# Performance work log

Hardware: AMD Instinct MI355X
Metric: run time of the kernel (lower is better)

## Reference

```python
import jax, jax.numpy as jnp
import numpy as np

N = 50000
E = 800000
IN_CH = 128
HIDDEN = 32
HEADS = 4
OUT_CH = 64
NEG_SLOPE = 0.2


def setup_inputs() -> dict:
    key = jax.random.key(0)
    ks = jax.random.split(key, 12)
    x = jax.random.normal(ks[0], (N, IN_CH), dtype=jnp.float32)
    edge_index = jax.random.randint(ks[1], (2, E), 0, N, dtype=jnp.int64)
    # layer 1: GATConv(IN_CH, HIDDEN, heads=4, concat=True)
    s1 = 1.0 / np.sqrt(IN_CH)
    W1 = jax.random.normal(ks[2], (IN_CH, HEADS * HIDDEN), dtype=jnp.float32) * s1
    att_src1 = jax.random.normal(ks[3], (HEADS, HIDDEN), dtype=jnp.float32) * 0.1
    att_dst1 = jax.random.normal(ks[4], (HEADS, HIDDEN), dtype=jnp.float32) * 0.1
    b1 = jnp.zeros((HEADS * HIDDEN,), dtype=jnp.float32)
    # layer 2: GATConv(HEADS*HIDDEN, OUT_CH, heads=1, concat=False)
    s2 = 1.0 / np.sqrt(HEADS * HIDDEN)
    W2 = jax.random.normal(ks[5], (HEADS * HIDDEN, OUT_CH), dtype=jnp.float32) * s2
    att_src2 = jax.random.normal(ks[6], (1, OUT_CH), dtype=jnp.float32) * 0.1
    att_dst2 = jax.random.normal(ks[7], (1, OUT_CH), dtype=jnp.float32) * 0.1
    b2 = jnp.zeros((OUT_CH,), dtype=jnp.float32)
    return {"x": x, "edge_index": edge_index, "W1": W1, "att_src1": att_src1,
            "att_dst1": att_dst1, "b1": b1, "W2": W2, "att_src2": att_src2,
            "att_dst2": att_dst2, "b2": b2}


def gat_conv(x, src, dst, W, a_src, a_dst, bias, heads, out_ch, concat):
    n = x.shape[0]
    h = (x @ W).reshape(n, heads, out_ch)               # [N, H, C]
    alpha_s = jnp.sum(h * a_src[None], axis=-1)          # [N, H]
    alpha_d = jnp.sum(h * a_dst[None], axis=-1)          # [N, H]
    e = alpha_s[src] + alpha_d[dst]                      # [E, H]
    e = jnp.where(e > 0, e, NEG_SLOPE * e)               # leaky_relu(0.2)
    # segment softmax over incoming edges of each dst node
    e_max = jax.ops.segment_max(e, dst, num_segments=n)
    e_max = jnp.where(jnp.isfinite(e_max), e_max, 0.0)
    ex = jnp.exp(e - e_max[dst])
    denom = jax.ops.segment_sum(ex, dst, num_segments=n)
    alpha = ex / (denom[dst] + 1e-16)                    # [E, H]
    msg = h[src] * alpha[:, :, None]                     # [E, H, C]
    out = jax.ops.segment_sum(msg, dst, num_segments=n)  # [N, H, C]
    if concat:
        out = out.reshape(n, heads * out_ch)
    else:
        out = out.mean(axis=1)
    return out + bias


def reference(x, edge_index, W1, att_src1, att_dst1, b1, W2, att_src2, att_dst2, b2):
    n = x.shape[0]
    loop = jnp.arange(n, dtype=edge_index.dtype)
    src = jnp.concatenate([edge_index[0], loop])  # add self-loops (PyG default)
    dst = jnp.concatenate([edge_index[1], loop])
    h = gat_conv(x, src, dst, W1, att_src1, att_dst1, b1, HEADS, HIDDEN, True)
    h = jax.nn.elu(h)
    return gat_conv(h, src, dst, W2, att_src2, att_dst2, b2, 1, OUT_CH, False)
```

## Files before the change

### kernel.cpp

```cpp
#include <hip/hip_runtime.h>

#define NN    50000
#define NE    800000
#define NET   850000
#define NBUCK ((NN + 255) / 256)
#define MAXB  8192

typedef __fp16 half2_t __attribute__((ext_vector_type(2)));
typedef _Float16 half8 __attribute__((ext_vector_type(8)));
typedef float floatx4 __attribute__((ext_vector_type(4)));

__device__ __forceinline__ float lrelu(float v) { return fmaxf(v, 0.2f * v); }
__device__ __forceinline__ unsigned pk16(float a, float b) {
    half2_t h = __builtin_amdgcn_cvt_pkrtz(a, b);
    return __builtin_bit_cast(unsigned, h);
}
__device__ __forceinline__ float2 unpk16(unsigned u) {
    half2_t h = __builtin_bit_cast(half2_t, u);
    return make_float2((float)h.x, (float)h.y);
}

__global__ void prep_w_kernel(const float* __restrict__ W1, const float* __restrict__ W2,
                              _Float16* __restrict__ w1t, _Float16* __restrict__ w2t)
{
    const int idx = blockIdx.x * 256 + threadIdx.x;
    if (idx < 16384) {
        const int k = idx >> 7, n = idx & 127;
        w1t[n * 128 + k] = (_Float16)W1[idx];
    } else {
        const int j = idx - 16384;
        const int k = j >> 6, n = j & 63;
        w2t[n * 128 + k] = (_Float16)W2[j];
    }
}

__global__ __launch_bounds__(256) void gemm1_mfma_kernel(
    const float* __restrict__ x, const _Float16* __restrict__ w1t,
    const float* __restrict__ att_s, const float* __restrict__ att_d,
    _Float16* __restrict__ h1h, float* __restrict__ as, float* __restrict__ ad)
{
    __shared__ _Float16 hs[64 * 128];
    const int t    = threadIdx.x;
    const int lane = t & 63;
    const int m    = lane & 15;
    const int q    = lane >> 4;
    const int wv   = t >> 6;
    const int gr0  = blockIdx.x * 64;
    const int rbase = gr0 + wv * 16;

    const int rme = rbase + m;
    const int rc  = rme < NN ? rme : NN - 1;
    const float* ap = x + (size_t)rc * 128 + q * 8;

    floatx4 acc[8];
#pragma unroll
    for (int nt = 0; nt < 8; nt++) acc[nt] = (floatx4){0.f, 0.f, 0.f, 0.f};

#pragma unroll
    for (int ks = 0; ks < 4; ks++) {
        const float4 f0 = *(const float4*)(ap + ks * 32);
        const float4 f1 = *(const float4*)(ap + ks * 32 + 4);
        const uint4 au = make_uint4(pk16(f0.x, f0.y), pk16(f0.z, f0.w),
                                    pk16(f1.x, f1.y), pk16(f1.z, f1.w));
        const half8 a = __builtin_bit_cast(half8, au);
#pragma unroll
        for (int nt = 0; nt < 8; nt++) {
            const half8 b = *(const half8*)(w1t + (nt * 16 + m) * 128 + ks * 32 + q * 8);
            acc[nt] = __builtin_amdgcn_mfma_f32_16x16x32_f16(a, b, acc[nt], 0, 0, 0);
        }
    }

    const int lrow0 = wv * 16 + q * 4;
#pragma unroll
    for (int nt = 0; nt < 8; nt++)
#pragma unroll
        for (int r = 0; r < 4; r++)
            hs[(lrow0 + r) * 128 + nt * 16 + m] = (_Float16)acc[nt][r];
    __syncthreads();

#pragma unroll
    for (int i = t; i < 1024; i += 256) {
        const int row = i >> 4;
        if (gr0 + row < NN)
            ((half8*)h1h)[(size_t)(gr0 + row) * 16 + (i & 15)] = ((const half8*)hs)[i];
    }

    const int arow = t >> 2, hd = t & 3;
    const int grow = gr0 + arow;
    float ps = 0.f, pd = 0.f;
    const half8*  hp8 = (const half8*)(hs + arow * 128 + hd * 32);
    const float4* s4  = (const float4*)(att_s + hd * 32);
    const float4* d4  = (const float4*)(att_d + hd * 32);
#pragma unroll
    for (int cc = 0; cc < 4; cc++) {
        const half8 hv = hp8[cc];
        const float4 a = s4[cc * 2], b = s4[cc * 2 + 1];
        const float4 c = d4[cc * 2], e = d4[cc * 2 + 1];
        ps += (float)hv[0]*a.x + (float)hv[1]*a.y + (float)hv[2]*a.z + (float)hv[3]*a.w
            + (float)hv[4]*b.x + (float)hv[5]*b.y + (float)hv[6]*b.z + (float)hv[7]*b.w;
        pd += (float)hv[0]*c.x + (float)hv[1]*c.y + (float)hv[2]*c.z + (float)hv[3]*c.w
            + (float)hv[4]*e.x + (float)hv[5]*e.y + (float)hv[6]*e.z + (float)hv[7]*e.w;
    }
    if (grow < NN) {
        as[grow * 4 + hd] = ps;
        ad[grow * 4 + hd] = pd;
    }
}

__global__ __launch_bounds__(256) void gemm2_mfma_kernel(
    const _Float16* __restrict__ ah, const _Float16* __restrict__ w2t,
    const float* __restrict__ att_s, const float* __restrict__ att_d,
    _Float16* __restrict__ h2h, float* __restrict__ as, float* __restrict__ ad)
{
    __shared__ _Float16 hs[64 * 64];
    const int t    = threadIdx.x;
    const int lane = t & 63;
    const int m    = lane & 15;
    const int q    = lane >> 4;
    const int wv   = t >> 6;
    const int gr0  = blockIdx.x * 64;
    const int rbase = gr0 + wv * 16;

    const int rme = rbase + m;
    const int rc  = rme < NN ? rme : NN - 1;
    const _Float16* ap = ah + (size_t)rc * 128 + q * 8;

    floatx4 acc[4];
#pragma unroll
    for (int nt = 0; nt < 4; nt++) acc[nt] = (floatx4){0.f, 0.f, 0.f, 0.f};

#pragma unroll
    for (int ks = 0; ks < 4; ks++) {
        const half8 a = *(const half8*)(ap + ks * 32);
#pragma unroll
        for (int nt = 0; nt < 4; nt++) {
            const half8 b = *(const half8*)(w2t + (nt * 16 + m) * 128 + ks * 32 + q * 8);
            acc[nt] = __builtin_amdgcn_mfma_f32_16x16x32_f16(a, b, acc[nt], 0, 0, 0);
        }
    }

    const int lrow0 = wv * 16 + q * 4;
#pragma unroll
    for (int nt = 0; nt < 4; nt++)
#pragma unroll
        for (int r = 0; r < 4; r++)
            hs[(lrow0 + r) * 64 + nt * 16 + m] = (_Float16)acc[nt][r];
    __syncthreads();

#pragma unroll
    for (int i = t; i < 512; i += 256) {
        const int row = i >> 3;
        if (gr0 + row < NN)
            ((half8*)h2h)[(size_t)(gr0 + row) * 8 + (i & 7)] = ((const half8*)hs)[i];
    }

    const int arow = t >> 2, sg = t & 3;
    const int grow = gr0 + arow;
    float ps = 0.f, pd = 0.f;
    const half8*  hp8 = (const half8*)(hs + arow * 64 + sg * 16);
    const float4* s4  = (const float4*)(att_s + sg * 16);
    const float4* d4  = (const float4*)(att_d + sg * 16);
#pragma unroll
    for (int cc = 0; cc < 2; cc++) {
        const half8 hv = hp8[cc];
        const float4 a = s4[cc * 2], b = s4[cc * 2 + 1];
        const float4 c = d4[cc * 2], e = d4[cc * 2 + 1];
        ps += (float)hv[0]*a.x + (float)hv[1]*a.y + (float)hv[2]*a.z + (float)hv[3]*a.w
            + (float)hv[4]*b.x + (float)hv[5]*b.y + (float)hv[6]*b.z + (float)hv[7]*b.w;
        pd += (float)hv[0]*c.x + (float)hv[1]*c.y + (float)hv[2]*c.z + (float)hv[3]*c.w
            + (float)hv[4]*e.x + (float)hv[5]*e.y + (float)hv[6]*e.z + (float)hv[7]*e.w;
    }
    ps += __shfl_down(ps, 2);  pd += __shfl_down(pd, 2);
    ps += __shfl_down(ps, 1);  pd += __shfl_down(pd, 1);
    if (sg == 0 && grow < NN) { as[grow] = ps; ad[grow] = pd; }
}

__global__ __launch_bounds__(1024) void bin_kernel(const int* __restrict__ ei,
                                                   int* __restrict__ bcnt,
                                                   uint2* __restrict__ pairs)
{
    __shared__ int hist[NBUCK], base[NBUCK], cur[NBUCK];
    const int t = threadIdx.x;
    if (t < NBUCK) { hist[t] = 0; cur[t] = 0; }
    __syncthreads();
    const int e = blockIdx.x * 1024 + t;
    int s = 0, d = 0, bk = 0;
    const bool ok = e < NET;
    if (ok) {
        if (e < NE) { s = ei[e]; d = ei[NE + e]; } else { s = d = e - NE; }
        bk = d >> 8;
        atomicAdd(&hist[bk], 1);
    }
    __syncthreads();
    if (t < NBUCK && hist[t]) base[t] = atomicAdd(&bcnt[t], hist[t]);
    __syncthreads();
    if (ok) {
        const int r = atomicAdd(&cur[bk], 1);
        pairs[(size_t)bk * MAXB + base[bk] + r] = make_uint2((unsigned)s, (unsigned)d);
    }
}

__global__ __launch_bounds__(512) void bsort_ew1_kernel(
    const int* __restrict__ bcnt, const uint2* __restrict__ pairs,
    const float* __restrict__ as1, const float* __restrict__ ad1,
    int* __restrict__ row_beg, int* __restrict__ row_end,
    int* __restrict__ col, int* __restrict__ cold, float4* __restrict__ ex1)
{
    __shared__ int hist[256], cur[256], sh[256];
    __shared__ int outl[MAXB];
    __shared__ int outd[MAXB];
    const int b = blockIdx.x, t = threadIdx.x;
    const int m = bcnt[b];
    const int gbase = b * MAXB;
    if (t < 256) hist[t] = 0;
    __syncthreads();
    for (int i = t; i < m; i += 512)
        atomicAdd(&hist[pairs[gbase + i].y & 255], 1);
    __syncthreads();
    if (t < 256) sh[t] = hist[t];
    __syncthreads();
#pragma unroll
    for (int off = 1; off < 256; off <<= 1) {
        int u = (t < 256 && t >= off) ? sh[t - off] : 0;
        __syncthreads();
        if (t < 256) sh[t] += u;
        __syncthreads();
    }
    if (t < 256) {
        const int ex = sh[t] - hist[t];
        cur[t] = ex;
        const int node = (b << 8) + t;
        if (node < NN) {
            row_beg[node] = gbase + ex;
            row_end[node] = gbase + ex + hist[t];
        }
    }
    __syncthreads();
    for (int i = t; i < m; i += 512) {
        const uint2 p = pairs[gbase + i];
        const int r = atomicAdd(&cur[p.y & 255], 1);
        outl[r] = (int)p.x;
        outd[r] = (int)p.y;
    }
    __syncthreads();
    for (int i = t; i < m; i += 512) {
        const int s = outl[i], dd = outd[i];
        col[gbase + i]  = s;
        cold[gbase + i] = dd;
        const float4 a = ((const float4*)as1)[s];
        const float4 bb = ((const float4*)ad1)[dd];
        float4 v;
        v.x = __expf(lrelu(a.x + bb.x));
        v.y = __expf(lrelu(a.y + bb.y));
        v.z = __expf(lrelu(a.z + bb.z));
        v.w = __expf(lrelu(a.w + bb.w));
        ex1[gbase + i] = v;
    }
}

__global__ void edge_w2_kernel(const int* __restrict__ bcnt,
                               const int* __restrict__ col, const int* __restrict__ cold,
                               const float* __restrict__ as, const float* __restrict__ ad,
                               float* __restrict__ ex)
{
    const int bk    = blockIdx.x >> 5;
    const int local = (blockIdx.x & 31) * 256 + threadIdx.x;
    if (local >= bcnt[bk]) return;
    const int j = bk * MAXB + local;
    ex[j] = __expf(lrelu(as[col[j]] + ad[cold[j]]));
}

__global__ __launch_bounds__(256) void agg1_fused_kernel(
    const int* __restrict__ row_beg, const int* __restrict__ row_end,
    const int* __restrict__ col, const unsigned* __restrict__ hh,
    const float* __restrict__ exw, const float* __restrict__ b1,
    unsigned* __restrict__ acth)
{
    const int d    = __builtin_amdgcn_readfirstlane((blockIdx.x * 256 + threadIdx.x) >> 6);
    const int lane = threadIdx.x & 63;
    const int head = lane >> 4;
    const int beg = row_beg[d], end = row_end[d];

    float acc0 = 0.f, acc1 = 0.f, den = 0.f;
    int j = beg;
    for (; j + 16 <= end; j += 16) {
        float    w[16];
        unsigned g[16];
#pragma unroll
        for (int k = 0; k < 16; k++) {
            const int s = col[j + k];
            w[k] = exw[(j + k) * 4 + head];
            g[k] = hh[s * 64 + lane];
        }
#pragma unroll
        for (int k = 0; k < 16; k++) {
            const float2 g2 = unpk16(g[k]);
            den  += w[k];
            acc0 += w[k] * g2.x;
            acc1 += w[k] * g2.y;
        }
    }
    for (; j + 4 <= end; j += 4) {
        float    w[4];
        unsigned g[4];
#pragma unroll
        for (int k = 0; k < 4; k++) {
            const int s = col[j + k];
            w[k] = exw[(j + k) * 4 + head];
            g[k] = hh[s * 64 + lane];
        }
#pragma unroll
        for (int k = 0; k < 4; k++) {
            const float2 g2 = unpk16(g[k]);
            den  += w[k];
            acc0 += w[k] * g2.x;
            acc1 += w[k] * g2.y;
        }
    }
    for (; j < end; j++) {
        const float w = exw[j * 4 + head];
        const float2 g2 = unpk16(hh[col[j] * 64 + lane]);
        den  += w;
        acc0 += w * g2.x;
        acc1 += w * g2.y;
    }
    const float2 bb  = ((const float2*)b1)[lane];
    const float  inv = 1.f / (den + 1e-16f);
    float v0 = acc0 * inv + bb.x;
    float v1 = acc1 * inv + bb.y;
    v0 = v0 > 0.f ? v0 : (__expf(v0) - 1.f);
    v1 = v1 > 0.f ? v1 : (__expf(v1) - 1.f);
    acth[d * 64 + lane] = pk16(v0, v1);
}

__global__ __launch_bounds__(256) void agg2_fused_kernel(
    const int* __restrict__ row_beg, const int* __restrict__ row_end,
    const int* __restrict__ col, const _Float16* __restrict__ h,
    const float* __restrict__ exw, const float* __restrict__ b2,
    float* __restrict__ out)
{
    const int d    = __builtin_amdgcn_readfirstlane((blockIdx.x * 256 + threadIdx.x) >> 6);
    const int lane = threadIdx.x & 63;
    const int beg = row_beg[d], end = row_end[d];

    float acc = 0.f, den = 0.f;
    int j = beg;
    for (; j + 16 <= end; j += 16) {
        float w[16], g[16];
#pragma unroll
        for (int k = 0; k < 16; k++) {
            const int s = col[j + k];
            w[k] = exw[j + k];
            g[k] = (float)h[s * 64 + lane];
        }
#pragma unroll
        for (int k = 0; k < 16; k++) {
            den += w[k];
            acc += w[k] * g[k];
        }
    }
    for (; j + 4 <= end; j += 4) {
        float w[4], g[4];
#pragma unroll
        for (int k = 0; k < 4; k++) {
            const int s = col[j + k];
            w[k] = exw[j + k];
            g[k] = (float)h[s * 64 + lane];
        }
#pragma unroll
        for (int k = 0; k < 4; k++) {
            den += w[k];
            acc += w[k] * g[k];
        }
    }
    for (; j < end; j++) {
        const float w = exw[j];
        den += w;
        acc += w * (float)h[col[j] * 64 + lane];
    }
    out[d * 64 + lane] = acc / (den + 1e-16f) + b2[lane];
}

extern "C" void kernel_launch(void* const* d_in, const int* in_sizes, int n_in,
                              void* d_out, int out_size, void* d_ws, size_t ws_size,
                              hipStream_t stream)
{
    const float* x    = (const float*)d_in[0];
    const int*   ei   = (const int*)  d_in[1];
    const float* W1   = (const float*)d_in[2];
    const float* at_s1= (const float*)d_in[3];
    const float* at_d1= (const float*)d_in[4];
    const float* b1   = (const float*)d_in[5];
    const float* W2   = (const float*)d_in[6];
    const float* at_s2= (const float*)d_in[7];
    const float* at_d2= (const float*)d_in[8];
    const float* b2   = (const float*)d_in[9];
    float*       out  = (float*)d_out;

    const size_t NPAD = (size_t)NBUCK * MAXB;

    float* fw   = (float*)d_ws;
    float* as1  = fw;
    float* ad1  = as1  + NN * 4;
    float* as2  = ad1  + NN * 4;
    float* ad2  = as2  + NN;
    float* ex1  = ad2  + NN;
    float* ex2  = ex1  + NPAD * 4;
    _Float16* h1h   = (_Float16*)(ex2 + NPAD);
    _Float16* act1h = h1h  + (size_t)NN * 128;
    _Float16* h2h   = act1h+ (size_t)NN * 128;
    _Float16* w1t   = h2h  + (size_t)NN * 64;
    _Float16* w2t   = w1t  + 16384;
    int*   row_beg = (int*)(w2t + 8192);
    int*   row_end = row_beg + NN;
    int*   col     = row_end + NN;
    int*   cold    = col  + NPAD;
    int*   bcnt    = cold + NPAD;
    uint2* pairs   = (uint2*)(bcnt + 256);

    hipMemsetAsync(bcnt, 0, 256 * sizeof(int), stream);

    const int eg1024 = (NET + 1023) / 1024;
    const int gemm_grid = (NN + 63) / 64;
    const int node_wave_grid = NN / 4;

    bin_kernel   <<<eg1024, 1024, 0, stream>>>(ei, bcnt, pairs);
    prep_w_kernel<<<96, 256, 0, stream>>>(W1, W2, w1t, w2t);

    gemm1_mfma_kernel<<<gemm_grid, 256, 0, stream>>>(x, w1t, at_s1, at_d1, h1h, as1, ad1);
    bsort_ew1_kernel <<<NBUCK, 512, 0, stream>>>(bcnt, pairs, as1, ad1,
                        row_beg, row_end, col, cold, (float4*)ex1);
    agg1_fused_kernel<<<node_wave_grid, 256, 0, stream>>>(row_beg, row_end, col,
                        (const unsigned*)h1h, ex1, b1, (unsigned*)act1h);

    gemm2_mfma_kernel<<<gemm_grid, 256, 0, stream>>>(act1h, w2t, at_s2, at_d2, h2h, as2, ad2);
    edge_w2_kernel   <<<NBUCK * 32, 256, 0, stream>>>(bcnt, col, cold, as2, ad2, ex2);
    agg2_fused_kernel<<<node_wave_grid, 256, 0, stream>>>(row_beg, row_end, col, h2h, ex2, b2, out);
}
```

Measured before the change: 224.3 us.

## Fuse edge attention weight computation into aggregation kernels and drop edge weight buffers

Edge attention weights are no longer precomputed into per-edge arrays (ex1, ex2) by the sort kernel and a separate edge kernel. Each aggregation wave now computes the weights for chunks of 64 incoming edges, using the source score and its own destination score, and stages them in per-wave shared memory. This removes one kernel launch, the cold array, and the per-edge weight writes and reads, and it lets the sort kernel run independently of gemm1. In exchange each aggregation wave does an extra gather of source scores plus exp work, and relies on an explicit lgkmcnt wait rather than a barrier for intra-wave LDS visibility.

```diff
diff --git a/kernel.cpp b/kernel.cpp
--- a/kernel.cpp
+++ b/kernel.cpp
@@ -200,15 +200,13 @@
     }
 }
 
-__global__ __launch_bounds__(512) void bsort_ew1_kernel(
+__global__ __launch_bounds__(512) void bsort_kernel(
     const int* __restrict__ bcnt, const uint2* __restrict__ pairs,
-    const float* __restrict__ as1, const float* __restrict__ ad1,
     int* __restrict__ row_beg, int* __restrict__ row_end,
-    int* __restrict__ col, int* __restrict__ cold, float4* __restrict__ ex1)
+    int* __restrict__ col)
 {
     __shared__ int hist[256], cur[256], sh[256];
     __shared__ int outl[MAXB];
-    __shared__ int outd[MAXB];
     const int b = blockIdx.x, t = threadIdx.x;
     const int m = bcnt[b];
     const int gbase = b * MAXB;
@@ -240,89 +238,85 @@
         const uint2 p = pairs[gbase + i];
         const int r = atomicAdd(&cur[p.y & 255], 1);
         outl[r] = (int)p.x;
-        outd[r] = (int)p.y;
-    }
-    __syncthreads();
-    for (int i = t; i < m; i += 512) {
-        const int s = outl[i], dd = outd[i];
-        col[gbase + i]  = s;
-        cold[gbase + i] = dd;
-        const float4 a = ((const float4*)as1)[s];
-        const float4 bb = ((const float4*)ad1)[dd];
-        float4 v;
-        v.x = __expf(lrelu(a.x + bb.x));
-        v.y = __expf(lrelu(a.y + bb.y));
-        v.z = __expf(lrelu(a.z + bb.z));
-        v.w = __expf(lrelu(a.w + bb.w));
-        ex1[gbase + i] = v;
-    }
-}
-
-__global__ void edge_w2_kernel(const int* __restrict__ bcnt,
-                               const int* __restrict__ col, const int* __restrict__ cold,
-                               const float* __restrict__ as, const float* __restrict__ ad,
-                               float* __restrict__ ex)
-{
-    const int bk    = blockIdx.x >> 5;
-    const int local = (blockIdx.x & 31) * 256 + threadIdx.x;
-    if (local >= bcnt[bk]) return;
-    const int j = bk * MAXB + local;
-    ex[j] = __expf(lrelu(as[col[j]] + ad[cold[j]]));
+    }
+    __syncthreads();
+    for (int i = t; i < m; i += 512) col[gbase + i] = outl[i];
 }
 
 __global__ __launch_bounds__(256) void agg1_fused_kernel(
     const int* __restrict__ row_beg, const int* __restrict__ row_end,
     const int* __restrict__ col, const unsigned* __restrict__ hh,
-    const float* __restrict__ exw, const float* __restrict__ b1,
-    unsigned* __restrict__ acth)
-{
+    const float* __restrict__ as1, const float* __restrict__ ad1,
+    const float* __restrict__ b1, unsigned* __restrict__ acth)
+{
+    __shared__ float wbuf[4][64 * 4];
+    const int wv   = threadIdx.x >> 6;
     const int d    = __builtin_amdgcn_readfirstlane((blockIdx.x * 256 + threadIdx.x) >> 6);
     const int lane = threadIdx.x & 63;
     const int head = lane >> 4;
     const int beg = row_beg[d], end = row_end[d];
+    const float4 ad4 = ((const float4*)ad1)[d];
+    float* wb = wbuf[wv];
 
     float acc0 = 0.f, acc1 = 0.f, den = 0.f;
-    int j = beg;
-    for (; j + 16 <= end; j += 16) {
-        float    w[16];
-        unsigned g[16];
-#pragma unroll
-        for (int k = 0; k < 16; k++) {
-            const int s = col[j + k];
-            w[k] = exw[(j + k) * 4 + head];
-            g[k] = hh[s * 64 + lane];
-        }
-#pragma unroll
-        for (int k = 0; k < 16; k++) {
-            const float2 g2 = unpk16(g[k]);
-            den  += w[k];
-            acc0 += w[k] * g2.x;
-            acc1 += w[k] * g2.y;
-        }
-    }
-    for (; j + 4 <= end; j += 4) {
-        float    w[4];
-        unsigned g[4];
-#pragma unroll
-        for (int k = 0; k < 4; k++) {
-            const int s = col[j + k];
-            w[k] = exw[(j + k) * 4 + head];
-            g[k] = hh[s * 64 + lane];
-        }
-#pragma unroll
-        for (int k = 0; k < 4; k++) {
-            const float2 g2 = unpk16(g[k]);
-            den  += w[k];
-            acc0 += w[k] * g2.x;
-            acc1 += w[k] * g2.y;
-        }
-    }
-    for (; j < end; j++) {
-        const float w = exw[j * 4 + head];
-        const float2 g2 = unpk16(hh[col[j] * 64 + lane]);
-        den  += w;
-        acc0 += w * g2.x;
-        acc1 += w * g2.y;
+
+    for (int jb = beg; jb < end; jb += 64) {
+        const int cnt = min(64, end - jb);
+        {
+            const int sl = col[jb + min(lane, cnt - 1)];
+            const float4 a = ((const float4*)as1)[sl];
+            float4 w4;
+            w4.x = __expf(lrelu(a.x + ad4.x));
+            w4.y = __expf(lrelu(a.y + ad4.y));
+            w4.z = __expf(lrelu(a.z + ad4.z));
+            w4.w = __expf(lrelu(a.w + ad4.w));
+            ((float4*)wb)[lane] = w4;
+        }
+        __asm__ volatile("s_waitcnt lgkmcnt(0)" ::: "memory");
+
+        int k = 0;
+        for (; k + 16 <= cnt; k += 16) {
+            float    w[16];
+            unsigned g[16];
+#pragma unroll
+            for (int u = 0; u < 16; u++) {
+                const int s = col[jb + k + u];
+                w[u] = wb[(k + u) * 4 + head];
+                g[u] = hh[s * 64 + lane];
+            }
+#pragma unroll
+            for (int u = 0; u < 16; u++) {
+                const float2 g2 = unpk16(g[u]);
+                den  += w[u];
+                acc0 += w[u] * g2.x;
+                acc1 += w[u] * g2.y;
+            }
+        }
+        for (; k + 4 <= cnt; k += 4) {
+            float    w[4];
+            unsigned g[4];
+#pragma unroll
+            for (int u = 0; u < 4; u++) {
+                const int s = col[jb + k + u];
+                w[u] = wb[(k + u) * 4 + head];
+                g[u] = hh[s * 64 + lane];
+            }
+#pragma unroll
+            for (int u = 0; u < 4; u++) {
+                const float2 g2 = unpk16(g[u]);
+                den  += w[u];
+                acc0 += w[u] * g2.x;
+                acc1 += w[u] * g2.y;
+            }
+        }
+        for (; k < cnt; k++) {
+            const float w = wb[k * 4 + head];
+            const float2 g2 = unpk16(hh[col[jb + k] * 64 + lane]);
+            den  += w;
+            acc0 += w * g2.x;
+            acc1 += w * g2.y;
+        }
+        __asm__ volatile("" ::: "memory");
     }
     const float2 bb  = ((const float2*)b1)[lane];
     const float  inv = 1.f / (den + 1e-16f);
@@ -336,47 +330,62 @@
 __global__ __launch_bounds__(256) void agg2_fused_kernel(
     const int* __restrict__ row_beg, const int* __restrict__ row_end,
     const int* __restrict__ col, const _Float16* __restrict__ h,
-    const float* __restrict__ exw, const float* __restrict__ b2,
-    float* __restrict__ out)
-{
+    const float* __restrict__ as2, const float* __restrict__ ad2,
+    const float* __restrict__ b2, float* __restrict__ out)
+{
+    __shared__ float wbuf[4][64];
+    const int wv   = threadIdx.x >> 6;
     const int d    = __builtin_amdgcn_readfirstlane((blockIdx.x * 256 + threadIdx.x) >> 6);
     const int lane = threadIdx.x & 63;
     const int beg = row_beg[d], end = row_end[d];
+    const float add = ad2[d];
+    float* wb = wbuf[wv];
 
     float acc = 0.f, den = 0.f;
-    int j = beg;
-    for (; j + 16 <= end; j += 16) {
-        float w[16], g[16];
-#pragma unroll
-        for (int k = 0; k < 16; k++) {
-            const int s = col[j + k];
-            w[k] = exw[j + k];
-            g[k] = (float)h[s * 64 + lane];
-        }
-#pragma unroll
-        for (int k = 0; k < 16; k++) {
-            den += w[k];
-            acc += w[k] * g[k];
-        }
-    }
-    for (; j + 4 <= end; j += 4) {
-        float w[4], g[4];
-#pragma unroll
-        for (int k = 0; k < 4; k++) {
-            const int s = col[j + k];
-            w[k] = exw[j + k];
-            g[k] = (float)h[s * 64 + lane];
-        }
-#pragma unroll
-        for (int k = 0; k < 4; k++) {
-            den += w[k];
-            acc += w[k] * g[k];
-        }
-    }
-    for (; j < end; j++) {
-        const float w = exw[j];
-        den += w;
-        acc += w * (float)h[col[j] * 64 + lane];
+
+    for (int jb = beg; jb < end; jb += 64) {
+        const int cnt = min(64, end - jb);
+        {
+            const int sl = col[jb + min(lane, cnt - 1)];
+            wb[lane] = __expf(lrelu(as2[sl] + add));
+        }
+        __asm__ volatile("s_waitcnt lgkmcnt(0)" ::: "memory");
+
+        int k = 0;
+        for (; k + 16 <= cnt; k += 16) {
+            float w[16], g[16];
+#pragma unroll
+            for (int u = 0; u < 16; u++) {
+                const int s = col[jb + k + u];
+                w[u] = wb[k + u];
+                g[u] = (float)h[s * 64 + lane];
+            }
+#pragma unroll
+            for (int u = 0; u < 16; u++) {
+                den += w[u];
+                acc += w[u] * g[u];
+            }
+        }
+        for (; k + 4 <= cnt; k += 4) {
+            float w[4], g[4];
+#pragma unroll
+            for (int u = 0; u < 4; u++) {
+                const int s = col[jb + k + u];
+                w[u] = wb[k + u];
+                g[u] = (float)h[s * 64 + lane];
+            }
+#pragma unroll
+            for (int u = 0; u < 4; u++) {
+                den += w[u];
+                acc += w[u] * g[u];
+            }
+        }
+        for (; k < cnt; k++) {
+            const float w = wb[k];
+            den += w;
+            acc += w * (float)h[col[jb + k] * 64 + lane];
+        }
+        __asm__ volatile("" ::: "memory");
     }
     out[d * 64 + lane] = acc / (den + 1e-16f) + b2[lane];
 }
@@ -404,9 +413,7 @@
     float* ad1  = as1  + NN * 4;
     float* as2  = ad1  + NN * 4;
     float* ad2  = as2  + NN;
-    float* ex1  = ad2  + NN;
-    float* ex2  = ex1  + NPAD * 4;
-    _Float16* h1h   = (_Float16*)(ex2 + NPAD);
+    _Float16* h1h   = (_Float16*)(ad2 + NN);
     _Float16* act1h = h1h  + (size_t)NN * 128;
     _Float16* h2h   = act1h+ (size_t)NN * 128;
     _Float16* w1t   = h2h  + (size_t)NN * 64;
@@ -414,8 +421,7 @@
     int*   row_beg = (int*)(w2t + 8192);
     int*   row_end = row_beg + NN;
     int*   col     = row_end + NN;
-    int*   cold    = col  + NPAD;
-    int*   bcnt    = cold + NPAD;
+    int*   bcnt    = col + NPAD;
     uint2* pairs   = (uint2*)(bcnt + 256);
 
     hipMemsetAsync(bcnt, 0, 256 * sizeof(int), stream);
@@ -426,14 +432,13 @@
 
     bin_kernel   <<<eg1024, 1024, 0, stream>>>(ei, bcnt, pairs);
     prep_w_kernel<<<96, 256, 0, stream>>>(W1, W2, w1t, w2t);
+    bsort_kernel <<<NBUCK, 512, 0, stream>>>(bcnt, pairs, row_beg, row_end, col);
 
     gemm1_mfma_kernel<<<gemm_grid, 256, 0, stream>>>(x, w1t, at_s1, at_d1, h1h, as1, ad1);
-    bsort_ew1_kernel <<<NBUCK, 512, 0, stream>>>(bcnt, pairs, as1, ad1,
-                        row_beg, row_end, col, cold, (float4*)ex1);
     agg1_fused_kernel<<<node_wave_grid, 256, 0, stream>>>(row_beg, row_end, col,
-                        (const unsigned*)h1h, ex1, b1, (unsigned*)act1h);
+                        (const unsigned*)h1h, as1, ad1, b1, (unsigned*)act1h);
 
     gemm2_mfma_kernel<<<gemm_grid, 256, 0, stream>>>(act1h, w2t, at_s2, at_d2, h2h, as2, ad2);
-    edge_w2_kernel   <<<NBUCK * 32, 256, 0, stream>>>(bcnt, col, cold, as2, ad2, ex2);
-    agg2_fused_kernel<<<node_wave_grid, 256, 0, stream>>>(row_beg, row_end, col, h2h, ex2, b2, out);
-}
+    agg2_fused_kernel<<<node_wave_grid, 256, 0, stream>>>(row_beg, row_end, col,
+                        h2h, as2, ad2, b2, out);
+}
```

Result: faster. 216.2 us (-3.6%).
